# Kernel tuning notes

Hardware: AMD Instinct MI355X
Metric: run time of the kernel (lower is better)

## Reference

```python
import jax, jax.numpy as jnp
import numpy as np

EPS = 1e-5

def _layernorm(x, w, b):
    mu = jnp.mean(x, axis=-1, keepdims=True)
    var = jnp.var(x, axis=-1, keepdims=True)
    return (x - mu) * jax.lax.rsqrt(var + EPS) * w + b

def setup_inputs() -> dict:
    key = jax.random.key(0)
    ks = jax.random.split(key, 9)
    b, s, dim = 4, 4096, 2048
    m, n, dim_ctx = 8, 64, 1024
    heads, dim_head = 8, 64
    inner = heads * dim_head
    x = jax.random.normal(ks[0], (b, s, dim), dtype=jnp.float32)
    context = jax.random.normal(ks[1], (b, m, n, dim_ctx), dtype=jnp.float32)
    media_locations = jax.random.randint(ks[2], (b, s), 0, m, dtype=jnp.int64)
    scale = 0.02
    norm_w = jnp.ones((dim,), jnp.float32)
    norm_b = jnp.zeros((dim,), jnp.float32)
    normc_w = jnp.ones((dim_ctx,), jnp.float32)
    normc_b = jnp.zeros((dim_ctx,), jnp.float32)
    Wq = jax.random.normal(ks[3], (dim, inner), jnp.float32) * scale
    Wkv = jax.random.normal(ks[4], (dim_ctx, 2 * inner), jnp.float32) * scale
    Wout = jax.random.normal(ks[5], (inner, dim), jnp.float32) * scale
    return {"x": x, "context": context, "media_locations": media_locations,
            "norm_w": norm_w, "norm_b": norm_b, "normc_w": normc_w, "normc_b": normc_b,
            "Wq": Wq, "Wkv": Wkv, "Wout": Wout}

def reference(x, context, media_locations, norm_w, norm_b, normc_w, normc_b, Wq, Wkv, Wout):
    heads, dim_head = 8, 64
    b, m, n, dc = context.shape
    scale = dim_head ** -0.5
    xn = _layernorm(x, norm_w, norm_b)                       # [b,s,dim]
    ctx = _layernorm(context.reshape(b, m * n, dc), normc_w, normc_b)  # [b,mn,dc]
    q = xn @ Wq                                              # [b,s,inner]
    kv = ctx @ Wkv                                           # [b,mn,2*inner]
    k, v = jnp.split(kv, 2, axis=-1)
    def to_heads(t):
        return t.reshape(t.shape[0], t.shape[1], heads, dim_head).transpose(0, 2, 1, 3)
    q, k, v = to_heads(q), to_heads(k), to_heads(v)          # [b,h,*,d]
    sim = jnp.einsum('bhid,bhjd->bhij', q, k) * scale        # [b,h,s,mn]
    # image-causal mask: kv token j belongs to image j//n; query i may only
    # attend to image media_locations[b,i] (negative index => all masked)
    j_img = jnp.arange(m * n) // n                           # [mn]
    allowed = (media_locations[:, :, None] == j_img[None, None, :]) & (media_locations[:, :, None] >= 0)
    sim = jnp.where(allowed[:, None, :, :], sim, -jnp.inf)
    attn = jax.nn.softmax(sim, axis=-1)
    out = jnp.einsum('bhij,bhjd->bhid', attn, v)             # [b,h,s,d]
    out = out.transpose(0, 2, 1, 3).reshape(b, x.shape[1], heads * dim_head)
    return out @ Wout
```

## Files before the change

kernel.cpp:

```cpp
#include <hip/hip_runtime.h>

typedef unsigned short u16;
typedef unsigned int u32;
typedef __attribute__((ext_vector_type(8))) short short8;
typedef __attribute__((ext_vector_type(4))) short short4_t;
typedef __attribute__((ext_vector_type(4))) float f32x4;

__device__ __forceinline__ float bf2f(u16 u){ return __uint_as_float(((u32)u)<<16); }
__device__ __forceinline__ u16 f2bf(float f){ u32 x = __float_as_uint(f); return (u16)((x + 0x7FFFu + ((x>>16)&1u)) >> 16); }

#define OFF_FLAG   ((size_t)0)
#define OFF_COUNTS ((size_t)256)
#define OFF_LISTS  ((size_t)4096)
#define OFF_XN     ((size_t)(1<<20))
#define OFF_CTXN   (OFF_XN    + (size_t)67108864)
#define OFF_WQT    (OFF_CTXN  + (size_t)4194304)
#define OFF_WKVT   (OFF_WQT   + (size_t)2097152)
#define OFF_WOUTT  (OFF_WKVT  + (size_t)2097152)
#define OFF_Q      (OFF_WOUTT + (size_t)2097152)
#define OFF_KV     (OFF_Q     + (size_t)16777216)
#define OFF_ATTN   (OFF_KV    + (size_t)4194304)
#define OFF_VT     (OFF_ATTN  + (size_t)16777216)
#define WS_NEEDED  (OFF_VT    + (size_t)2097152)

__global__ void prep_kernel(const int* __restrict__ ml32, int* __restrict__ flag, int* __restrict__ counts){
  int t = threadIdx.x;
  if (t < 32) counts[t] = 0;
  __shared__ int nz;
  if (t == 0) nz = 0;
  __syncthreads();
  if (t < 128 && ml32[2*t+1] != 0) atomicAdd(&nz, 1);
  __syncthreads();
  if (t == 0) flag[0] = (nz == 0) ? 1 : 0;
}

template<int D>
__global__ __launch_bounds__(256) void ln_bf16(const float* __restrict__ x, const float* __restrict__ w,
                                               const float* __restrict__ b, u16* __restrict__ out){
  constexpr int VEC = D/256;
  int row = blockIdx.x;
  const float* xr = x + (size_t)row*D;
  int tid = threadIdx.x;
  float v[VEC];
  #pragma unroll
  for (int i=0;i<VEC;i+=4){
    f32x4 f = *(const f32x4*)(xr + tid*VEC + i);
    v[i]=f[0]; v[i+1]=f[1]; v[i+2]=f[2]; v[i+3]=f[3];
  }
  float s=0.f, sq=0.f;
  #pragma unroll
  for (int i=0;i<VEC;++i){ s += v[i]; sq += v[i]*v[i]; }
  #pragma unroll
  for (int off=32;off;off>>=1){ s += __shfl_xor(s,off,64); sq += __shfl_xor(sq,off,64); }
  __shared__ float red[8];
  int lane = tid&63, wid = tid>>6;
  if (lane==0){ red[wid]=s; red[4+wid]=sq; }
  __syncthreads();
  s  = red[0]+red[1]+red[2]+red[3];
  sq = red[4]+red[5]+red[6]+red[7];
  float mu = s/(float)D;
  float var = sq/(float)D - mu*mu;
  float rs = rsqrtf(var + 1e-5f);
  u16 o[VEC];
  #pragma unroll
  for (int i=0;i<VEC;i+=4){
    f32x4 wv = *(const f32x4*)(w + tid*VEC + i);
    f32x4 bv = *(const f32x4*)(b + tid*VEC + i);
    #pragma unroll
    for (int u=0;u<4;++u) o[i+u] = f2bf((v[i+u]-mu)*rs*wv[u] + bv[u]);
  }
  if constexpr (VEC==8) *(short8*)(out + (size_t)row*D + tid*8) = *(short8*)o;
  else                  *(short4_t*)(out + (size_t)row*D + tid*4) = *(short4_t*)o;
}

__global__ __launch_bounds__(256) void transpose_w(const float* __restrict__ in, u16* __restrict__ out, int K, int N){
  __shared__ float t[32][33];
  int tx = threadIdx.x, ty = threadIdx.y;
  int n0 = blockIdx.x*32, k0 = blockIdx.y*32;
  #pragma unroll
  for (int r=0;r<32;r+=8) t[ty+r][tx] = in[(size_t)(k0+ty+r)*N + n0+tx];
  __syncthreads();
  #pragma unroll
  for (int r=0;r<32;r+=8) out[(size_t)(n0+ty+r)*K + k0+tx] = f2bf(t[tx][ty+r]);
}

__global__ __launch_bounds__(256) void transpose_v(const u16* __restrict__ kvb, u16* __restrict__ vt){
  int h = blockIdx.x, bl = blockIdx.y;
  __shared__ u16 t[64][72];
  int tid = threadIdx.x;
  const u16* src = kvb + (size_t)(bl*64)*1024 + 512 + h*64;
  #pragma unroll
  for (int i=0;i<2;++i){
    int idx = i*2048 + tid*8;
    int key = idx>>6, d = idx&63;
    *(short8*)&t[key][d] = *(const short8*)(src + (size_t)key*1024 + d);
  }
  __syncthreads();
  u16* dst = vt + (size_t)(bl*8+h)*4096;
  #pragma unroll
  for (int i=0;i<2;++i){
    int idx = i*2048 + tid*8;
    int d = idx>>6, k0 = idx&63;
    u16 tmp[8];
    #pragma unroll
    for (int u=0;u<8;++u) tmp[u] = t[k0+u][d];
    *(short8*)(dst + d*64 + k0) = *(short8*)tmp;
  }
}

template<int MODE>
__global__ __launch_bounds__(256) void gemm_bt(const u16* __restrict__ A, const u16* __restrict__ B,
                                               void* __restrict__ Cv, int M, int N, int K){
  __shared__ __align__(16) u16 lds[2][2][128*32];
  int tid = threadIdx.x, lane = tid&63, wid = tid>>6;
  int nbn = N>>7;
  int nwg = gridDim.x;
  int wg = blockIdx.x;
  int cpx = nwg>>3;
  wg = (wg&7)*cpx + (wg>>3);
  int brow = wg/nbn, bcol = wg%nbn;

  auto stage = [&](int buf, int kt){
    #pragma unroll
    for (int i=0;i<2;++i){
      int cb = i*256 + wid*64;
      int c  = cb + lane;
      int row = c>>2, kc = c&3;
      const u16* ga = A + (size_t)(brow*128+row)*K + kt*32 + kc*8;
      __builtin_amdgcn_global_load_lds((const __attribute__((address_space(1))) u32*)ga,
          (__attribute__((address_space(3))) u32*)&lds[buf][0][cb*8], 16, 0, 0);
      const u16* gb = B + (size_t)(bcol*128+row)*K + kt*32 + kc*8;
      __builtin_amdgcn_global_load_lds((const __attribute__((address_space(1))) u32*)gb,
          (__attribute__((address_space(3))) u32*)&lds[buf][1][cb*8], 16, 0, 0);
    }
  };

  int wm = wid>>1, wn = wid&1;
  f32x4 acc[4][4] = {};
  int nkt = K>>5;
  stage(0,0);
  __syncthreads();
  for (int kt=0; kt<nkt; ++kt){
    int cur = kt&1;
    if (kt+1<nkt) stage(cur^1, kt+1);
    short8 af[4], bfr[4];
    int r = lane&15, kq = lane>>4;
    #pragma unroll
    for (int mi=0;mi<4;++mi) af[mi]  = *(const short8*)&lds[cur][0][(wm*64+mi*16+r)*32 + kq*8];
    #pragma unroll
    for (int ni=0;ni<4;++ni) bfr[ni] = *(const short8*)&lds[cur][1][(wn*64+ni*16+r)*32 + kq*8];
    #pragma unroll
    for (int mi=0;mi<4;++mi)
      #pragma unroll
      for (int ni=0;ni<4;++ni)
        acc[mi][ni] = __builtin_amdgcn_mfma_f32_16x16x32_bf16(af[mi], bfr[ni], acc[mi][ni], 0,0,0);
    __syncthreads();
  }
  int r4 = (lane>>4)*4, cc = lane&15;
  #pragma unroll
  for (int mi=0;mi<4;++mi)
    #pragma unroll
    for (int ni=0;ni<4;++ni)
      #pragma unroll
      for (int rr=0;rr<4;++rr){
        int row = brow*128 + wm*64 + mi*16 + r4 + rr;
        int col = bcol*128 + wn*64 + ni*16 + cc;
        float val = acc[mi][ni][rr];
        if (MODE==2) val *= 0.125f;
        if (MODE)  ((u16*)Cv)[(size_t)row*N+col] = f2bf(val);
        else       ((float*)Cv)[(size_t)row*N+col] = val;
      }
}

__global__ void bucket_kernel(const int* __restrict__ ml32, const int* __restrict__ flag,
                              int* __restrict__ counts, int* __restrict__ lists){
  int i = blockIdx.x*256 + threadIdx.x;
  int loc = flag[0] ? ml32[2*i] : ml32[i];
  int bl = (i>>12)*8 + loc;
  int pos = atomicAdd(&counts[bl], 1);
  lists[bl*4096 + pos] = i & 4095;
}

__global__ __launch_bounds__(256) void attn_mfma(const u16* __restrict__ qb, const u16* __restrict__ kvb,
                                                 const u16* __restrict__ vt, u16* __restrict__ ob,
                                                 const int* __restrict__ counts, const int* __restrict__ lists){
  int bl = blockIdx.z, hg = blockIdx.y, chunk = blockIdx.x;
  int cnt = counts[bl];
  int q0 = chunk*64;
  if (q0 >= cnt) return;
  int b = bl>>3, loc = bl&7;
  int tid = threadIdx.x, lane = tid&63, wid = tid>>6;
  int h = hg*4 + wid;
  __shared__ u16 plds[4][64][72];

  int r = lane&15, g = lane>>4;

  int qidx[4];
  #pragma unroll
  for (int mt=0;mt<4;++mt){
    int p = q0 + mt*16 + r;
    qidx[mt] = (p < cnt) ? lists[bl*4096 + p] : -1;
  }

  short8 qf[4][2];
  #pragma unroll
  for (int mt=0;mt<4;++mt){
    int qi = qidx[mt] < 0 ? 0 : qidx[mt];
    const u16* qrow = qb + ((size_t)(b*4096) + qi)*512 + h*64;
    qf[mt][0] = *(const short8*)(qrow + g*8);
    qf[mt][1] = *(const short8*)(qrow + 32 + g*8);
  }
  const u16* kbase = kvb + (size_t)(b*512 + loc*64)*1024 + h*64;
  short8 kfr[4][2];
  #pragma unroll
  for (int nt=0;nt<4;++nt){
    const u16* krow = kbase + (size_t)(nt*16 + r)*1024;
    kfr[nt][0] = *(const short8*)(krow + g*8);
    kfr[nt][1] = *(const short8*)(krow + 32 + g*8);
  }

  f32x4 acc[4][4] = {};
  #pragma unroll
  for (int mt=0;mt<4;++mt)
    #pragma unroll
    for (int nt=0;nt<4;++nt){
      acc[mt][nt] = __builtin_amdgcn_mfma_f32_16x16x32_bf16(qf[mt][0], kfr[nt][0], acc[mt][nt], 0,0,0);
      acc[mt][nt] = __builtin_amdgcn_mfma_f32_16x16x32_bf16(qf[mt][1], kfr[nt][1], acc[mt][nt], 0,0,0);
    }

  #pragma unroll
  for (int mt=0;mt<4;++mt){
    #pragma unroll
    for (int rr=0;rr<4;++rr){
      float m = fmaxf(fmaxf(acc[mt][0][rr], acc[mt][1][rr]), fmaxf(acc[mt][2][rr], acc[mt][3][rr]));
      #pragma unroll
      for (int off=1;off<16;off<<=1) m = fmaxf(m, __shfl_xor(m, off));
      float e0 = __expf(acc[mt][0][rr]-m), e1 = __expf(acc[mt][1][rr]-m);
      float e2 = __expf(acc[mt][2][rr]-m), e3 = __expf(acc[mt][3][rr]-m);
      float sum = (e0+e1)+(e2+e3);
      #pragma unroll
      for (int off=1;off<16;off<<=1) sum += __shfl_xor(sum, off);
      float rs = 1.0f/sum;
      int row = mt*16 + g*4 + rr;
      plds[wid][row][ 0 + r] = f2bf(e0*rs);
      plds[wid][row][16 + r] = f2bf(e1*rs);
      plds[wid][row][32 + r] = f2bf(e2*rs);
      plds[wid][row][48 + r] = f2bf(e3*rs);
    }
  }

  const u16* vbase = vt + (size_t)(bl*8 + h)*4096;
  short8 vf[2][4];
  #pragma unroll
  for (int nt=0;nt<4;++nt){
    const u16* vrow = vbase + (size_t)(nt*16 + r)*64;
    vf[0][nt] = *(const short8*)(vrow + g*8);
    vf[1][nt] = *(const short8*)(vrow + 32 + g*8);
  }

  #pragma unroll
  for (int mt=0;mt<4;++mt)
    #pragma unroll
    for (int nt=0;nt<4;++nt)
      acc[mt][nt] = (f32x4){0.f,0.f,0.f,0.f};
  #pragma unroll
  for (int mt=0;mt<4;++mt){
    short8 pa0 = *(const short8*)&plds[wid][mt*16 + r][g*8];
    short8 pa1 = *(const short8*)&plds[wid][mt*16 + r][32 + g*8];
    #pragma unroll
    for (int nt=0;nt<4;++nt){
      acc[mt][nt] = __builtin_amdgcn_mfma_f32_16x16x32_bf16(pa0, vf[0][nt], acc[mt][nt], 0,0,0);
      acc[mt][nt] = __builtin_amdgcn_mfma_f32_16x16x32_bf16(pa1, vf[1][nt], acc[mt][nt], 0,0,0);
    }
  }

  #pragma unroll
  for (int mt=0;mt<4;++mt){
    #pragma unroll
    for (int rr=0;rr<4;++rr){
      int qrow = __shfl(qidx[mt], g*4 + rr, 16);
      if (qrow >= 0){
        u16* orow = ob + ((size_t)(b*4096) + qrow)*512 + h*64;
        #pragma unroll
        for (int nt=0;nt<4;++nt) orow[nt*16 + r] = f2bf(acc[mt][nt][rr]);
      }
    }
  }
}

extern "C" void kernel_launch(void* const* d_in, const int* in_sizes, int n_in,
                              void* d_out, int out_size, void* d_ws, size_t ws_size,
                              hipStream_t stream) {
  const float* x    = (const float*)d_in[0];
  const float* ctx  = (const float*)d_in[1];
  const int*   ml   = (const int*)d_in[2];
  const float* nw   = (const float*)d_in[3];
  const float* nb   = (const float*)d_in[4];
  const float* ncw  = (const float*)d_in[5];
  const float* ncb  = (const float*)d_in[6];
  const float* Wq   = (const float*)d_in[7];
  const float* Wkv  = (const float*)d_in[8];
  const float* Wout = (const float*)d_in[9];
  float* out = (float*)d_out;
  char* ws = (char*)d_ws;
  if (ws_size < WS_NEEDED) return;

  int* flag   = (int*)(ws + OFF_FLAG);
  int* counts = (int*)(ws + OFF_COUNTS);
  int* lists  = (int*)(ws + OFF_LISTS);
  u16* xn     = (u16*)(ws + OFF_XN);
  u16* ctxn   = (u16*)(ws + OFF_CTXN);
  u16* WqT    = (u16*)(ws + OFF_WQT);
  u16* WkvT   = (u16*)(ws + OFF_WKVT);
  u16* WoutT  = (u16*)(ws + OFF_WOUTT);
  u16* qbuf   = (u16*)(ws + OFF_Q);
  u16* kvbuf  = (u16*)(ws + OFF_KV);
  u16* attn_o = (u16*)(ws + OFF_ATTN);
  u16* vtbuf  = (u16*)(ws + OFF_VT);

  prep_kernel<<<1,256,0,stream>>>(ml, flag, counts);
  ln_bf16<2048><<<16384,256,0,stream>>>(x,   nw,  nb,  xn);
  ln_bf16<1024><<<2048, 256,0,stream>>>(ctx, ncw, ncb, ctxn);
  transpose_w<<<dim3(16,64), dim3(32,8),0,stream>>>(Wq,   WqT,   2048, 512);
  transpose_w<<<dim3(32,32), dim3(32,8),0,stream>>>(Wkv,  WkvT,  1024, 1024);
  transpose_w<<<dim3(64,16), dim3(32,8),0,stream>>>(Wout, WoutT, 512,  2048);
  gemm_bt<2><<<512, 256,0,stream>>>(xn,   WqT,  qbuf,  16384, 512,  2048);
  gemm_bt<1><<<128, 256,0,stream>>>(ctxn, WkvT, kvbuf, 2048,  1024, 1024);
  transpose_v<<<dim3(8,32),256,0,stream>>>(kvbuf, vtbuf);
  bucket_kernel<<<64,256,0,stream>>>(ml, flag, counts, lists);
  attn_mfma<<<dim3(64,2,32),256,0,stream>>>(qbuf, kvbuf, vtbuf, attn_o, counts, lists);
  gemm_bt<0><<<2048,256,0,stream>>>(attn_o, WoutT, out, 16384, 2048, 512);
}
```

Before: 244.8 us.

## Stage gathered Q rows and outputs through LDS with all heads per block

The attention kernel now runs 8 waves per block, one per head, over 32 query rows instead of 4 heads over 64 rows. Gathered Q rows are loaded as full 1 KB rows with coalesced 16-byte loads into shared memory, and output is staged in LDS and written back as full contiguous rows. This replaces the scattered per-head 16-byte reads and 2-byte output stores. The cost is more shared memory, extra barriers and more blocks with half the query tile each. The attention kernel is only part of a pipeline that is dominated by the GEMMs.

```diff
diff --git a/kernel.cpp b/kernel.cpp
--- a/kernel.cpp
+++ b/kernel.cpp
@@ -181,35 +181,46 @@
   lists[bl*4096 + pos] = i & 4095;
 }
 
-__global__ __launch_bounds__(256) void attn_mfma(const u16* __restrict__ qb, const u16* __restrict__ kvb,
-                                                 const u16* __restrict__ vt, u16* __restrict__ ob,
-                                                 const int* __restrict__ counts, const int* __restrict__ lists){
-  int bl = blockIdx.z, hg = blockIdx.y, chunk = blockIdx.x;
+__global__ __launch_bounds__(512) void attn_mfma2(const u16* __restrict__ qb, const u16* __restrict__ kvb,
+                                                  const u16* __restrict__ vt, u16* __restrict__ ob,
+                                                  const int* __restrict__ counts, const int* __restrict__ lists){
+  int bl = blockIdx.y, chunk = blockIdx.x;
   int cnt = counts[bl];
-  int q0 = chunk*64;
+  int q0 = chunk*32;
   if (q0 >= cnt) return;
   int b = bl>>3, loc = bl&7;
-  int tid = threadIdx.x, lane = tid&63, wid = tid>>6;
-  int h = hg*4 + wid;
-  __shared__ u16 plds[4][64][72];
+  int tid = threadIdx.x, lane = tid&63, h = tid>>6;
+  __shared__ u16 qs[32][520];
+  __shared__ u16 plds[8][32][72];
+  __shared__ int qi[32];
+
+  if (tid < 32){
+    int p = q0 + tid;
+    qi[tid] = (p < cnt) ? lists[bl*4096 + p] : -1;
+  }
+  __syncthreads();
+
+  const u16* qbase = qb + (size_t)(b*4096)*512;
+  #pragma unroll
+  for (int p=0;p<4;++p){
+    int c = p*512 + tid;
+    int row = c>>6, cc = c&63;
+    int qq = qi[row];
+    if (qq >= 0)
+      *(short8*)&qs[row][cc*8] = *(const short8*)(qbase + (size_t)qq*512 + cc*8);
+  }
+  __syncthreads();
 
   int r = lane&15, g = lane>>4;
 
-  int qidx[4];
-  #pragma unroll
-  for (int mt=0;mt<4;++mt){
-    int p = q0 + mt*16 + r;
-    qidx[mt] = (p < cnt) ? lists[bl*4096 + p] : -1;
-  }
-
-  short8 qf[4][2];
-  #pragma unroll
-  for (int mt=0;mt<4;++mt){
-    int qi = qidx[mt] < 0 ? 0 : qidx[mt];
-    const u16* qrow = qb + ((size_t)(b*4096) + qi)*512 + h*64;
-    qf[mt][0] = *(const short8*)(qrow + g*8);
-    qf[mt][1] = *(const short8*)(qrow + 32 + g*8);
-  }
+  short8 qf[2][2];
+  #pragma unroll
+  for (int mt=0;mt<2;++mt){
+    qf[mt][0] = *(const short8*)&qs[mt*16+r][h*64 + g*8];
+    qf[mt][1] = *(const short8*)&qs[mt*16+r][h*64 + 32 + g*8];
+  }
+  __syncthreads();
+
   const u16* kbase = kvb + (size_t)(b*512 + loc*64)*1024 + h*64;
   short8 kfr[4][2];
   #pragma unroll
@@ -219,9 +230,9 @@
     kfr[nt][1] = *(const short8*)(krow + 32 + g*8);
   }
 
-  f32x4 acc[4][4] = {};
-  #pragma unroll
-  for (int mt=0;mt<4;++mt)
+  f32x4 acc[2][4] = {};
+  #pragma unroll
+  for (int mt=0;mt<2;++mt)
     #pragma unroll
     for (int nt=0;nt<4;++nt){
       acc[mt][nt] = __builtin_amdgcn_mfma_f32_16x16x32_bf16(qf[mt][0], kfr[nt][0], acc[mt][nt], 0,0,0);
@@ -229,7 +240,7 @@
     }
 
   #pragma unroll
-  for (int mt=0;mt<4;++mt){
+  for (int mt=0;mt<2;++mt){
     #pragma unroll
     for (int rr=0;rr<4;++rr){
       float m = fmaxf(fmaxf(acc[mt][0][rr], acc[mt][1][rr]), fmaxf(acc[mt][2][rr], acc[mt][3][rr]));
@@ -242,10 +253,10 @@
       for (int off=1;off<16;off<<=1) sum += __shfl_xor(sum, off);
       float rs = 1.0f/sum;
       int row = mt*16 + g*4 + rr;
-      plds[wid][row][ 0 + r] = f2bf(e0*rs);
-      plds[wid][row][16 + r] = f2bf(e1*rs);
-      plds[wid][row][32 + r] = f2bf(e2*rs);
-      plds[wid][row][48 + r] = f2bf(e3*rs);
+      plds[h][row][ 0 + r] = f2bf(e0*rs);
+      plds[h][row][16 + r] = f2bf(e1*rs);
+      plds[h][row][32 + r] = f2bf(e2*rs);
+      plds[h][row][48 + r] = f2bf(e3*rs);
     }
   }
 
@@ -258,33 +269,37 @@
     vf[1][nt] = *(const short8*)(vrow + 32 + g*8);
   }
 
-  #pragma unroll
-  for (int mt=0;mt<4;++mt)
-    #pragma unroll
-    for (int nt=0;nt<4;++nt)
-      acc[mt][nt] = (f32x4){0.f,0.f,0.f,0.f};
-  #pragma unroll
-  for (int mt=0;mt<4;++mt){
-    short8 pa0 = *(const short8*)&plds[wid][mt*16 + r][g*8];
-    short8 pa1 = *(const short8*)&plds[wid][mt*16 + r][32 + g*8];
+  f32x4 oacc[2][4] = {};
+  #pragma unroll
+  for (int mt=0;mt<2;++mt){
+    short8 pa0 = *(const short8*)&plds[h][mt*16 + r][g*8];
+    short8 pa1 = *(const short8*)&plds[h][mt*16 + r][32 + g*8];
     #pragma unroll
     for (int nt=0;nt<4;++nt){
-      acc[mt][nt] = __builtin_amdgcn_mfma_f32_16x16x32_bf16(pa0, vf[0][nt], acc[mt][nt], 0,0,0);
-      acc[mt][nt] = __builtin_amdgcn_mfma_f32_16x16x32_bf16(pa1, vf[1][nt], acc[mt][nt], 0,0,0);
-    }
-  }
-
-  #pragma unroll
-  for (int mt=0;mt<4;++mt){
+      oacc[mt][nt] = __builtin_amdgcn_mfma_f32_16x16x32_bf16(pa0, vf[0][nt], oacc[mt][nt], 0,0,0);
+      oacc[mt][nt] = __builtin_amdgcn_mfma_f32_16x16x32_bf16(pa1, vf[1][nt], oacc[mt][nt], 0,0,0);
+    }
+  }
+
+  #pragma unroll
+  for (int mt=0;mt<2;++mt)
     #pragma unroll
     for (int rr=0;rr<4;++rr){
-      int qrow = __shfl(qidx[mt], g*4 + rr, 16);
-      if (qrow >= 0){
-        u16* orow = ob + ((size_t)(b*4096) + qrow)*512 + h*64;
-        #pragma unroll
-        for (int nt=0;nt<4;++nt) orow[nt*16 + r] = f2bf(acc[mt][nt][rr]);
-      }
-    }
+      int row = mt*16 + g*4 + rr;
+      #pragma unroll
+      for (int nt=0;nt<4;++nt)
+        qs[row][h*64 + nt*16 + r] = f2bf(oacc[mt][nt][rr]);
+    }
+  __syncthreads();
+
+  u16* obase = ob + (size_t)(b*4096)*512;
+  #pragma unroll
+  for (int p=0;p<4;++p){
+    int c = p*512 + tid;
+    int row = c>>6, cc = c&63;
+    int qq = qi[row];
+    if (qq >= 0)
+      *(short8*)(obase + (size_t)qq*512 + cc*8) = *(const short8*)&qs[row][cc*8];
   }
 }
 
@@ -328,6 +343,6 @@
   gemm_bt<1><<<128, 256,0,stream>>>(ctxn, WkvT, kvbuf, 2048,  1024, 1024);
   transpose_v<<<dim3(8,32),256,0,stream>>>(kvbuf, vtbuf);
   bucket_kernel<<<64,256,0,stream>>>(ml, flag, counts, lists);
-  attn_mfma<<<dim3(64,2,32),256,0,stream>>>(qbuf, kvbuf, vtbuf, attn_o, counts, lists);
+  attn_mfma2<<<dim3(128,32),512,0,stream>>>(qbuf, kvbuf, vtbuf, attn_o, counts, lists);
   gemm_bt<0><<<2048,256,0,stream>>>(attn_o, WoutT, out, 16384, 2048, 512);
 }
```

Result: faster. 237.4 us (-3.0%).
